# Performance work log

Hardware: AMD Instinct MI355X
Metric: run time of the kernel (lower is better)

## Reference

```python
import jax, jax.numpy as jnp
import numpy as np

VOCAB = 50257
D = 256
N_UTT = 64
L = 512


def gru_scan(x, W_ih, W_hh, b_ih, b_hh):
    # torch nn.GRU (single layer, batch_first) semantics.
    # x: [B, T, d] -> outputs [B, T, d]
    B, T, d = x.shape
    gx = jnp.einsum('btd,gd->btg', x, W_ih) + b_ih  # [B, T, 3d] input gates precomputed
    gx = jnp.transpose(gx, (1, 0, 2))               # [T, B, 3d] for scan over time

    def step(h, gxt):
        gh = h @ W_hh.T + b_hh                      # [B, 3d]
        xr, xz, xn = jnp.split(gxt, 3, axis=-1)
        hr, hz, hn = jnp.split(gh, 3, axis=-1)
        r = jax.nn.sigmoid(xr + hr)
        z = jax.nn.sigmoid(xz + hz)
        n = jnp.tanh(xn + r * hn)
        h_new = (1.0 - z) * n + z * h
        return h_new, h_new

    h0 = jnp.zeros((B, d), x.dtype)
    _, hs = jax.lax.scan(step, h0, gx)              # hs: [T, B, d]
    return jnp.transpose(hs, (1, 0, 2))


def attn_pool(out, w, b):
    # out: [B, T, d]; Linear(d,1) -> softmax over T -> weighted sum
    logits = out @ w + b                            # [B, T]
    weights = jax.nn.softmax(logits, axis=-1)
    return jnp.einsum('bt,btd->bd', weights, out)   # [B, d]


def setup_inputs() -> dict:
    key = jax.random.key(0)
    ks = jax.random.split(key, 16)
    s = 1.0 / np.sqrt(D)
    u = lambda k, shape: jax.random.uniform(k, shape, jnp.float32, -s, s)
    return {
        'tokens': jax.random.randint(ks[0], (N_UTT, L), 0, VOCAB, dtype=jnp.int32),
        'embed': jax.random.normal(ks[1], (VOCAB, D), jnp.float32),
        'wg_Wih': u(ks[2], (3 * D, D)),
        'wg_Whh': u(ks[3], (3 * D, D)),
        'wg_bih': u(ks[4], (3 * D,)),
        'wg_bhh': u(ks[5], (3 * D,)),
        'ua_w': u(ks[6], (D,)),
        'ua_b': u(ks[7], ()),
        'sg_Wih': u(ks[8], (3 * D, D)),
        'sg_Whh': u(ks[9], (3 * D, D)),
        'sg_bih': u(ks[10], (3 * D,)),
        'sg_bhh': u(ks[11], (3 * D,)),
        'da_w': u(ks[12], (D,)),
        'da_b': u(ks[13], ()),
    }


def reference(tokens, embed, wg_Wih, wg_Whh, wg_bih, wg_bhh, ua_w, ua_b,
              sg_Wih, sg_Whh, sg_bih, sg_bhh, da_w, da_b):
    # Word level: embed each utterance, GRU, attention pooling (batched over utterances)
    emb = embed[tokens]                                   # [N, L, d]
    word_out = gru_scan(emb, wg_Wih, wg_Whh, wg_bih, wg_bhh)
    utt_vecs = attn_pool(word_out, ua_w, ua_b)            # [N, d]
    # Sentence level: pad_sequence of [1,d] vectors -> [N, 1, d] (batch=N, seq=1)
    sent_in = utt_vecs[:, None, :]                        # [N, 1, d]
    sent_out = gru_scan(sent_in, sg_Wih, sg_Whh, sg_bih, sg_bhh)
    dialog_vec = attn_pool(sent_out, da_w, da_b)          # [N, d] (softmax over seq len 1)
    return dialog_vec
```

## Files before the change

kernel.cpp:

```cpp
#include <hip/hip_runtime.h>

typedef _Float16 f16x8 __attribute__((ext_vector_type(8)));
typedef float f32x4 __attribute__((ext_vector_type(4)));

constexpr int D = 256;
constexpr int NUTT = 64;
constexpr int L = 512;
constexpr int G = 768;
constexpr int NBLK = 6;
constexpr int NPROD = 192;
constexpr int NJOBS = 8 * NUTT * NBLK;

__device__ __forceinline__ void lds_barrier() {
  asm volatile("s_waitcnt lgkmcnt(0)\n\ts_barrier" ::: "memory");
}

__device__ __forceinline__ float fast_rcp(float x) {
  return __builtin_amdgcn_rcpf(x);
}
__device__ __forceinline__ float sigm(float x) {
  return fast_rcp(1.0f + __expf(-x));
}
__device__ __forceinline__ float tanh_f(float x) {
  float ax = fabsf(x);
  float e = __expf(-2.0f * ax);
  float r = (1.0f - e) * fast_rcp(1.0f + e);
  return copysignf(r, x);
}

__device__ __constant__ int c_chunk_of_rb[8] = {0, 1, 2, 2, 3, 3, 4, 4};

__global__ __launch_bounds__(256) void pack_wih(
    const float* __restrict__ Wih, _Float16* __restrict__ hi,
    _Float16* __restrict__ lo, int* cnt) {
  if (blockIdx.x == 0) {
    cnt[threadIdx.x << 4] = 0;
    cnt[(threadIdx.x + 256) << 4] = 0;
  }
  const int d = blockIdx.x * 256 + threadIdx.x;
  const int j = d & 7;
  const int l15 = (d >> 3) & 15;
  const int lk = (d >> 7) & 3;
  const int f = (d >> 9) & 7;
  const int it = d >> 12;
  const int g = 16 * it + l15;
  const int k = 32 * f + 8 * lk + j;
  float v = Wih[g * 256 + k];
  _Float16 h = (_Float16)v;
  hi[d] = h;
  lo[d] = (_Float16)(v - (float)h);
}

__global__ __launch_bounds__(512, 2) void hran_mega(
    const int* __restrict__ tokens, const float* __restrict__ embed,
    const _Float16* __restrict__ whi, const _Float16* __restrict__ wlo,
    const float* __restrict__ bih,
    const float* __restrict__ Whh,
    const float* __restrict__ bhh,
    const float* __restrict__ uaw,
    const float* __restrict__ sWih, const float* __restrict__ sbih,
    const float* __restrict__ sbhh,
    float* __restrict__ gx,
    _Float16* __restrict__ wo16,
    int* cnt,
    float* __restrict__ out) {
  __shared__ __align__(16) _Float16 hbuf[2][D];
  __shared__ float pre[3][D];
  __shared__ float lg[L];
  __shared__ float red[16];
  __shared__ float part[D];
  __shared__ __align__(16) float ut[D];

  const int bx = blockIdx.x;
  const int t = threadIdx.x;
  const int w = t >> 6;
  const int lane = t & 63;
  const int l15 = lane & 15;
  const int lk = lane >> 4;

  if (bx >= NUTT) {
    const int p = bx - NUTT;
    const f16x8* Bh = (const f16x8*)whi;
    const f16x8* Bl = (const f16x8*)wlo;
    const int fragbase = lk * 16 + l15;
    const int wr = w & 3;
    const int wc = w >> 2;

    for (int J = p; J < NJOBS; J += NPROD) {
      const int rb = J / (NUTT * NBLK);
      const int rem = J % (NUTT * NBLK);
      const int u = rem / NBLK;
      const int nb = rem % NBLK;
      const int m0 = u * L + rb * 64;
      const int n0 = nb * 128 + wc * 64;
      const int it0 = nb * 8 + wc * 4;

      const int tok = tokens[m0 + 16 * wr + l15];
      const float* arow = embed + (size_t)tok * D;

      f32x4 acc[4] = {};
#pragma unroll
      for (int f = 0; f < 8; ++f) {
        const float* ap = arow + 32 * f + 8 * lk;
        float4 v0 = *(const float4*)(ap);
        float4 v1 = *(const float4*)(ap + 4);
        float av[8] = {v0.x, v0.y, v0.z, v0.w, v1.x, v1.y, v1.z, v1.w};
        f16x8 ahi, alo;
#pragma unroll
        for (int j = 0; j < 8; ++j) {
          _Float16 h = (_Float16)av[j];
          ahi[j] = h;
          alo[j] = (_Float16)(av[j] - (float)h);
        }
#pragma unroll
        for (int i = 0; i < 4; ++i) {
          const int frag = ((it0 + i) * 8 + f) * 64 + fragbase;
          f16x8 bhi = Bh[frag];
          f16x8 blo = Bl[frag];
          acc[i] = __builtin_amdgcn_mfma_f32_16x16x32_f16(ahi, bhi, acc[i], 0, 0, 0);
          acc[i] = __builtin_amdgcn_mfma_f32_16x16x32_f16(alo, bhi, acc[i], 0, 0, 0);
          acc[i] = __builtin_amdgcn_mfma_f32_16x16x32_f16(ahi, blo, acc[i], 0, 0, 0);
        }
      }
#pragma unroll
      for (int i = 0; i < 4; ++i) {
        const int n = n0 + 16 * i + l15;
        const float bb = bih[n];
#pragma unroll
        for (int reg = 0; reg < 4; ++reg) {
          const int m = m0 + 16 * wr + 4 * lk + reg;
          gx[(size_t)m * G + n] = acc[i][reg] + bb;
        }
      }
      __syncthreads();
      if (t == 0)
        __hip_atomic_fetch_add(&cnt[((u << 3) + c_chunk_of_rb[rb]) << 4], 1,
                               __ATOMIC_RELEASE, __HIP_MEMORY_SCOPE_AGENT);
    }
    return;
  }

  const int b = bx;

  f16x8 Bf[6][8];
#pragma unroll
  for (int i = 0; i < 6; ++i) {
    const float* row = Whh + (size_t)(96 * w + 16 * i + l15) * D + 8 * lk;
#pragma unroll
    for (int f = 0; f < 8; ++f) {
      float4 v0 = *(const float4*)(row + 32 * f);
      float4 v1 = *(const float4*)(row + 32 * f + 4);
      Bf[i][f] = f16x8{(_Float16)v0.x, (_Float16)v0.y,
                       (_Float16)v0.z, (_Float16)v0.w,
                       (_Float16)v1.x, (_Float16)v1.y,
                       (_Float16)v1.z, (_Float16)v1.w};
    }
  }

  float bR = 0.0f, bZ = 0.0f, bN = 0.0f;
  float gr = 0.0f, gz = 0.0f, gn = 0.0f;
  float hprev = 0.0f;
  float* gxb = gx + (size_t)b * L * G;
  _Float16* wob = wo16 + (size_t)b * L * D;
  if (t < 256) {
    bR = bhh[t]; bZ = bhh[D + t]; bN = bhh[2 * D + t];
    hbuf[0][t] = (_Float16)0.0f;
  }
  __syncthreads();

  const int cstart[5] = {0, 64, 128, 256, 384};
  const int csize[5]  = {64, 64, 128, 128, 128};
  const int cneed[5]  = {6, 6, 12, 12, 12};

  for (int c = 0; c < 5; ++c) {
    if (t == 0) {
      while (__hip_atomic_load(&cnt[((b << 3) + c) << 4],
                               __ATOMIC_ACQUIRE,
                               __HIP_MEMORY_SCOPE_AGENT) < cneed[c])
        __builtin_amdgcn_s_sleep(8);
    }
    __syncthreads();
    __threadfence();
    if (t < 256) {
      const float* gc = gxb + (size_t)cstart[c] * G;
      gr = gc[t]; gz = gc[D + t]; gn = gc[2 * D + t];
    }

    const int cs = csize[c];
    for (int tsl = 0; tsl < cs; ++tsl) {
      const int ts = cstart[c] + tsl;
      const int cur = ts & 1;
      const _Float16* hb = hbuf[cur];
      f16x8 A[8];
#pragma unroll
      for (int f = 0; f < 8; ++f)
        A[f] = *(const f16x8*)(hb + 32 * f + 8 * lk);

#pragma unroll
      for (int i = 0; i < 6; ++i) {
        f32x4 acc = {0.0f, 0.0f, 0.0f, 0.0f};
#pragma unroll
        for (int f = 0; f < 8; ++f)
          acc = __builtin_amdgcn_mfma_f32_16x16x32_f16(A[f], Bf[i][f], acc,
                                                       0, 0, 0);
        if (lk == 0) {
          const int n = 96 * w + 16 * i + l15;
          pre[n >> 8][n & 255] = acc[0];
        }
      }
      lds_barrier();

      if (t < 256) {
        float aR = pre[0][t], aZ = pre[1][t], aNp = pre[2][t];
        float r = sigm(gr + aR + bR);
        float z = sigm(gz + aZ + bZ);
        float nn = tanh_f(gn + r * (aNp + bN));
        float hn = fmaf(z, hprev - nn, nn);
        hprev = hn;
        _Float16 hf = (_Float16)hn;
        hbuf[cur ^ 1][t] = hf;
        wob[(size_t)ts * D + t] = hf;
        if (tsl + 1 < cs) {
          const float* gxn = gxb + (size_t)(ts + 1) * G;
          gr = gxn[t]; gz = gxn[D + t]; gn = gxn[2 * D + t];
        }
      }
      lds_barrier();
    }
  }

  asm volatile("s_waitcnt vmcnt(0)" ::: "memory");
  __syncthreads();

  {
    const float ua0 = uaw[lane], ua1 = uaw[lane + 64];
    const float ua2 = uaw[lane + 128], ua3 = uaw[lane + 192];
    for (int r = 0; r < 64; ++r) {
      const int tt = 64 * w + r;
      const _Float16* row = wob + (size_t)tt * D;
      float p = (float)row[lane] * ua0 + (float)row[lane + 64] * ua1 +
                (float)row[lane + 128] * ua2 + (float)row[lane + 192] * ua3;
#pragma unroll
      for (int off = 32; off; off >>= 1) p += __shfl_down(p, off);
      if (lane == 0) lg[tt] = p;
    }
  }
  __syncthreads();

  {
    float v = lg[t];
    float m = v;
#pragma unroll
    for (int off = 32; off; off >>= 1) m = fmaxf(m, __shfl_xor(m, off));
    if (lane == 0) red[w] = m;
    __syncthreads();
    m = red[0];
#pragma unroll
    for (int i = 1; i < 8; ++i) m = fmaxf(m, red[i]);
    float e = __expf(v - m);
    float s = e;
#pragma unroll
    for (int off = 32; off; off >>= 1) s += __shfl_xor(s, off);
    if (lane == 0) red[8 + w] = s;
    __syncthreads();
    s = red[8];
#pragma unroll
    for (int i = 9; i < 16; ++i) s += red[i];
    lg[t] = e * (1.0f / s);
  }
  __syncthreads();

  {
    const int d = t & 255, half = t >> 8;
    float acc = 0.0f;
    const _Float16* bbp = wob + (size_t)half * 256 * D;
    const float* lgh = lg + half * 256;
#pragma unroll 4
    for (int k = 0; k < 256; ++k)
      acc = fmaf(lgh[k], (float)bbp[(size_t)k * D + d], acc);
    if (half == 1) part[d] = acc;
    __syncthreads();
    if (half == 0) ut[d] = acc + part[d];
    __syncthreads();
  }

  if (t < 256) {
    const int d = t;
    const float* wr = sWih + (size_t)d * D;
    const float* wz = sWih + (size_t)(D + d) * D;
    const float* wn = sWih + (size_t)(2 * D + d) * D;
    float ar = 0.0f, az = 0.0f, an = 0.0f;
    for (int k = 0; k < D; k += 4) {
      float4 vr = *(const float4*)(wr + k);
      float4 vz = *(const float4*)(wz + k);
      float4 vn = *(const float4*)(wn + k);
      float u0 = ut[k], u1 = ut[k + 1], u2 = ut[k + 2], u3 = ut[k + 3];
      ar += vr.x * u0 + vr.y * u1 + vr.z * u2 + vr.w * u3;
      az += vz.x * u0 + vz.y * u1 + vz.z * u2 + vz.w * u3;
      an += vn.x * u0 + vn.y * u1 + vn.z * u2 + vn.w * u3;
    }
    float r = sigm(ar + sbih[d] + sbhh[d]);
    float z = sigm(az + sbih[D + d] + sbhh[D + d]);
    float n = tanh_f(an + sbih[2 * D + d] + r * sbhh[2 * D + d]);
    out[(size_t)b * D + d] = (1.0f - z) * n;
  }
}

extern "C" void kernel_launch(void* const* d_in, const int* in_sizes, int n_in,
                              void* d_out, int out_size, void* d_ws, size_t ws_size,
                              hipStream_t stream) {
  const int* tokens    = (const int*)d_in[0];
  const float* embed   = (const float*)d_in[1];
  const float* wg_Wih  = (const float*)d_in[2];
  const float* wg_Whh  = (const float*)d_in[3];
  const float* wg_bih  = (const float*)d_in[4];
  const float* wg_bhh  = (const float*)d_in[5];
  const float* ua_w    = (const float*)d_in[6];
  const float* sg_Wih  = (const float*)d_in[8];
  const float* sg_bih  = (const float*)d_in[10];
  const float* sg_bhh  = (const float*)d_in[11];
  float* out = (float*)d_out;

  char* ws = (char*)d_ws;
  const size_t GXB = (size_t)NUTT * L * G * 4;
  float* gx = (float*)ws;
  _Float16* whi = (_Float16*)(ws + GXB);
  _Float16* wlo = whi + (size_t)G * D;
  int* cnt = (int*)(ws + GXB + (size_t)2 * G * D * 2);
  _Float16* wo16 = (_Float16*)(ws + GXB + (size_t)2 * G * D * 2 + 32768);

  pack_wih<<<G, 256, 0, stream>>>(wg_Wih, whi, wlo, cnt);
  hran_mega<<<NUTT + NPROD, 512, 0, stream>>>(
      tokens, embed, whi, wlo, wg_bih, wg_Whh, wg_bhh, ua_w,
      sg_Wih, sg_bih, sg_bhh, gx, wo16, cnt, out);
}
```

Before: 853.0 us.

## Launch one producer block per GEMM job, pad LDS to one block per CU, prefetch gx two steps ahead

Producer blocks no longer loop over jobs in a persistent grid; the grid now has one block per input-projection job (NJOBS), relying on the hardware scheduler. A large dummy LDS array plus launch_bounds(512,1) forces one block per CU, so the 64 recurrent blocks get a CU to themselves instead of sharing with producer blocks. The recurrent loop double-buffers the gx gate inputs in registers, loading two timesteps ahead to hide global-load latency. The risk is that recurrent blocks may not be scheduled before producers fill the machine. Fewer producers then run concurrently, and if the recurrent blocks were not resident a producer-consumer deadlock would be possible.

```diff
diff --git a/kernel.cpp b/kernel.cpp
--- a/kernel.cpp
+++ b/kernel.cpp
@@ -8,7 +8,6 @@
 constexpr int L = 512;
 constexpr int G = 768;
 constexpr int NBLK = 6;
-constexpr int NPROD = 192;
 constexpr int NJOBS = 8 * NUTT * NBLK;
 
 __device__ __forceinline__ void lds_barrier() {
@@ -51,7 +50,7 @@
   lo[d] = (_Float16)(v - (float)h);
 }
 
-__global__ __launch_bounds__(512, 2) void hran_mega(
+__global__ __launch_bounds__(512, 1) void hran_mega(
     const int* __restrict__ tokens, const float* __restrict__ embed,
     const _Float16* __restrict__ whi, const _Float16* __restrict__ wlo,
     const float* __restrict__ bih,
@@ -70,73 +69,72 @@
   __shared__ float red[16];
   __shared__ float part[D];
   __shared__ __align__(16) float ut[D];
+  __shared__ __align__(16) char lds_pad[76800];
 
   const int bx = blockIdx.x;
   const int t = threadIdx.x;
+  if (t == 0) ((volatile char*)lds_pad)[0] = 1;
   const int w = t >> 6;
   const int lane = t & 63;
   const int l15 = lane & 15;
   const int lk = lane >> 4;
 
   if (bx >= NUTT) {
-    const int p = bx - NUTT;
+    const int gbx = bx - NUTT;
+    const int rb = gbx / (NUTT * NBLK);
+    const int rem = gbx % (NUTT * NBLK);
+    const int u = rem / NBLK;
+    const int nb = rem % NBLK;
+    const int m0 = u * L + rb * 64;
+    const int wr = w & 3;
+    const int wc = w >> 2;
+    const int n0 = nb * 128 + wc * 64;
+    const int it0 = nb * 8 + wc * 4;
+
+    const int tok = tokens[m0 + 16 * wr + l15];
+    const float* arow = embed + (size_t)tok * D;
     const f16x8* Bh = (const f16x8*)whi;
     const f16x8* Bl = (const f16x8*)wlo;
     const int fragbase = lk * 16 + l15;
-    const int wr = w & 3;
-    const int wc = w >> 2;
-
-    for (int J = p; J < NJOBS; J += NPROD) {
-      const int rb = J / (NUTT * NBLK);
-      const int rem = J % (NUTT * NBLK);
-      const int u = rem / NBLK;
-      const int nb = rem % NBLK;
-      const int m0 = u * L + rb * 64;
-      const int n0 = nb * 128 + wc * 64;
-      const int it0 = nb * 8 + wc * 4;
-
-      const int tok = tokens[m0 + 16 * wr + l15];
-      const float* arow = embed + (size_t)tok * D;
-
-      f32x4 acc[4] = {};
-#pragma unroll
-      for (int f = 0; f < 8; ++f) {
-        const float* ap = arow + 32 * f + 8 * lk;
-        float4 v0 = *(const float4*)(ap);
-        float4 v1 = *(const float4*)(ap + 4);
-        float av[8] = {v0.x, v0.y, v0.z, v0.w, v1.x, v1.y, v1.z, v1.w};
-        f16x8 ahi, alo;
-#pragma unroll
-        for (int j = 0; j < 8; ++j) {
-          _Float16 h = (_Float16)av[j];
-          ahi[j] = h;
-          alo[j] = (_Float16)(av[j] - (float)h);
-        }
-#pragma unroll
-        for (int i = 0; i < 4; ++i) {
-          const int frag = ((it0 + i) * 8 + f) * 64 + fragbase;
-          f16x8 bhi = Bh[frag];
-          f16x8 blo = Bl[frag];
-          acc[i] = __builtin_amdgcn_mfma_f32_16x16x32_f16(ahi, bhi, acc[i], 0, 0, 0);
-          acc[i] = __builtin_amdgcn_mfma_f32_16x16x32_f16(alo, bhi, acc[i], 0, 0, 0);
-          acc[i] = __builtin_amdgcn_mfma_f32_16x16x32_f16(ahi, blo, acc[i], 0, 0, 0);
-        }
+
+    f32x4 acc[4] = {};
+#pragma unroll
+    for (int f = 0; f < 8; ++f) {
+      const float* ap = arow + 32 * f + 8 * lk;
+      float4 v0 = *(const float4*)(ap);
+      float4 v1 = *(const float4*)(ap + 4);
+      float av[8] = {v0.x, v0.y, v0.z, v0.w, v1.x, v1.y, v1.z, v1.w};
+      f16x8 ahi, alo;
+#pragma unroll
+      for (int j = 0; j < 8; ++j) {
+        _Float16 h = (_Float16)av[j];
+        ahi[j] = h;
+        alo[j] = (_Float16)(av[j] - (float)h);
       }
 #pragma unroll
       for (int i = 0; i < 4; ++i) {
-        const int n = n0 + 16 * i + l15;
-        const float bb = bih[n];
-#pragma unroll
-        for (int reg = 0; reg < 4; ++reg) {
-          const int m = m0 + 16 * wr + 4 * lk + reg;
-          gx[(size_t)m * G + n] = acc[i][reg] + bb;
-        }
-      }
-      __syncthreads();
-      if (t == 0)
-        __hip_atomic_fetch_add(&cnt[((u << 3) + c_chunk_of_rb[rb]) << 4], 1,
-                               __ATOMIC_RELEASE, __HIP_MEMORY_SCOPE_AGENT);
-    }
+        const int frag = ((it0 + i) * 8 + f) * 64 + fragbase;
+        f16x8 bhi = Bh[frag];
+        f16x8 blo = Bl[frag];
+        acc[i] = __builtin_amdgcn_mfma_f32_16x16x32_f16(ahi, bhi, acc[i], 0, 0, 0);
+        acc[i] = __builtin_amdgcn_mfma_f32_16x16x32_f16(alo, bhi, acc[i], 0, 0, 0);
+        acc[i] = __builtin_amdgcn_mfma_f32_16x16x32_f16(ahi, blo, acc[i], 0, 0, 0);
+      }
+    }
+#pragma unroll
+    for (int i = 0; i < 4; ++i) {
+      const int n = n0 + 16 * i + l15;
+      const float bb = bih[n];
+#pragma unroll
+      for (int reg = 0; reg < 4; ++reg) {
+        const int m = m0 + 16 * wr + 4 * lk + reg;
+        gx[(size_t)m * G + n] = acc[i][reg] + bb;
+      }
+    }
+    __syncthreads();
+    if (t == 0)
+      __hip_atomic_fetch_add(&cnt[((u << 3) + c_chunk_of_rb[rb]) << 4], 1,
+                             __ATOMIC_RELEASE, __HIP_MEMORY_SCOPE_AGENT);
     return;
   }
 
@@ -158,7 +156,8 @@
   }
 
   float bR = 0.0f, bZ = 0.0f, bN = 0.0f;
-  float gr = 0.0f, gz = 0.0f, gn = 0.0f;
+  float gAr = 0.f, gAz = 0.f, gAn = 0.f;
+  float gBr = 0.f, gBz = 0.f, gBn = 0.f;
   float hprev = 0.0f;
   float* gxb = gx + (size_t)b * L * G;
   _Float16* wob = wo16 + (size_t)b * L * D;
@@ -181,14 +180,17 @@
     }
     __syncthreads();
     __threadfence();
+    const int ts0 = cstart[c];
+    const int cs = csize[c];
     if (t < 256) {
-      const float* gc = gxb + (size_t)cstart[c] * G;
-      gr = gc[t]; gz = gc[D + t]; gn = gc[2 * D + t];
-    }
-
-    const int cs = csize[c];
+      const float* g0 = gxb + (size_t)ts0 * G;
+      gAr = g0[t]; gAz = g0[D + t]; gAn = g0[2 * D + t];
+      const float* g1 = gxb + (size_t)(ts0 + 1) * G;
+      gBr = g1[t]; gBz = g1[D + t]; gBn = g1[2 * D + t];
+    }
+
     for (int tsl = 0; tsl < cs; ++tsl) {
-      const int ts = cstart[c] + tsl;
+      const int ts = ts0 + tsl;
       const int cur = ts & 1;
       const _Float16* hb = hbuf[cur];
       f16x8 A[8];
@@ -211,6 +213,10 @@
       lds_barrier();
 
       if (t < 256) {
+        const bool odd = (tsl & 1) != 0;
+        float gr = odd ? gBr : gAr;
+        float gz = odd ? gBz : gAz;
+        float gn = odd ? gBn : gAn;
         float aR = pre[0][t], aZ = pre[1][t], aNp = pre[2][t];
         float r = sigm(gr + aR + bR);
         float z = sigm(gz + aZ + bZ);
@@ -220,9 +226,10 @@
         _Float16 hf = (_Float16)hn;
         hbuf[cur ^ 1][t] = hf;
         wob[(size_t)ts * D + t] = hf;
-        if (tsl + 1 < cs) {
-          const float* gxn = gxb + (size_t)(ts + 1) * G;
-          gr = gxn[t]; gz = gxn[D + t]; gn = gxn[2 * D + t];
+        if (tsl + 2 < cs) {
+          const float* gxn = gxb + (size_t)(ts + 2) * G;
+          if (odd) { gBr = gxn[t]; gBz = gxn[D + t]; gBn = gxn[2 * D + t]; }
+          else     { gAr = gxn[t]; gAz = gxn[D + t]; gAn = gxn[2 * D + t]; }
         }
       }
       lds_barrier();
@@ -330,7 +337,7 @@
   _Float16* wo16 = (_Float16*)(ws + GXB + (size_t)2 * G * D * 2 + 32768);
 
   pack_wih<<<G, 256, 0, stream>>>(wg_Wih, whi, wlo, cnt);
-  hran_mega<<<NUTT + NPROD, 512, 0, stream>>>(
+  hran_mega<<<NUTT + NJOBS, 512, 0, stream>>>(
       tokens, embed, whi, wlo, wg_bih, wg_Whh, wg_bhh, ua_w,
       sg_Wih, sg_bih, sg_bhh, gx, wo16, cnt, out);
 }
```

New measurement: 991.8 us. +16.3%, slower.
